# Kernel optimization log

Measured on AMD Instinct MI355X. Metric: run time of the kernel, lower is better.

The kernel has to match this reference:

```python
import jax, jax.numpy as jnp
import numpy as np

NUM_HEADS = 12
KEEP_RATE = 0.7


def setup_inputs() -> dict:
    key = jax.random.key(0)
    ks = jax.random.split(key, 5)
    B, N, C = 64, 197, 768
    x = jax.random.normal(ks[0], (B, N, C), dtype=jnp.float32)
    qkv_w = jax.random.normal(ks[1], (3 * C, C), dtype=jnp.float32) * (C ** -0.5)
    qkv_b = jax.random.normal(ks[2], (3 * C,), dtype=jnp.float32) * 0.02
    proj_w = jax.random.normal(ks[3], (C, C), dtype=jnp.float32) * (C ** -0.5)
    proj_b = jax.random.normal(ks[4], (C,), dtype=jnp.float32) * 0.02
    return {"x": x, "qkv_w": qkv_w, "qkv_b": qkv_b, "proj_w": proj_w, "proj_b": proj_b}


def reference(x, qkv_w, qkv_b, proj_w, proj_b):
    B, N, C = x.shape
    H = NUM_HEADS
    D = C // H
    scale = D ** -0.5
    # qkv projection: [B,N,3C] -> [3,B,H,N,D]
    qkv = (x @ qkv_w.T + qkv_b).reshape(B, N, 3, H, D).transpose(2, 0, 3, 1, 4)
    q, k, v = qkv[0], qkv[1], qkv[2]
    # full materialized attention (required for cls-row extraction)
    attn = jax.nn.softmax(jnp.einsum('bhqd,bhkd->bhqk', q, k) * scale, axis=-1)
    out = jnp.einsum('bhqk,bhkd->bqhd', attn, v).reshape(B, N, C)
    out = out @ proj_w.T + proj_b
    # EViT token pruning: cls-token attention over non-cls keys, head-averaged
    left_tokens = int(KEEP_RATE * (N - 1))  # 137
    cls_attn = attn[:, :, 0, 1:].mean(axis=1)  # [B, N-1]
    _, idx = jax.lax.top_k(cls_attn, left_tokens)  # sorted descending, like torch.topk
    index = jnp.broadcast_to(idx[:, :, None], (B, left_tokens, C))
    return (out, index, idx, cls_attn)
```

## Files before the change

### kernel.cpp

```cpp
#include <hip/hip_runtime.h>
#include <hip/hip_bf16.h>
#include <stdint.h>

constexpr int BATCH = 64;
constexpr int NTOK  = 197;
constexpr int CDIM  = 768;
constexpr int NH    = 12;
constexpr int HD    = 64;
constexpr int MROWS = BATCH * NTOK;
constexpr int MPAD  = 12800;
constexpr int NROWT = MPAD / 128;
constexpr int LEFT  = 137;
constexpr int KPAD  = 224;
constexpr int BH    = BATCH * NH;
constexpr int SPAD  = 208;

constexpr size_t OUT_OFF_OUT   = 0;
constexpr size_t OUT_OFF_INDEX = (size_t)BATCH * NTOK * CDIM;
constexpr size_t OUT_OFF_IDX   = OUT_OFF_INDEX + (size_t)BATCH * LEFT * CDIM;
constexpr size_t OUT_OFF_CLS   = OUT_OFF_IDX + (size_t)BATCH * LEFT;

constexpr size_t WS_CLSPH = 0;
constexpr size_t WS_CLSF  = WS_CLSPH + (size_t)BH * (NTOK - 1);
constexpr size_t WS_IDXI  = WS_CLSF  + (size_t)BATCH * (NTOK - 1);
constexpr size_t WS_Q0    = WS_IDXI  + (size_t)BATCH * LEFT;
constexpr size_t WS_XB    = WS_Q0  + (size_t)BATCH * CDIM;
constexpr size_t WS_WB    = WS_XB  + (size_t)MPAD * CDIM / 2;
constexpr size_t WS_PB    = WS_WB  + (size_t)3 * CDIM * CDIM / 2;
constexpr size_t WS_QB    = WS_PB  + (size_t)CDIM * CDIM / 2;
constexpr size_t WS_KB    = WS_QB  + (size_t)BH * NTOK * HD / 2;
constexpr size_t WS_VTB   = WS_KB  + (size_t)BH * NTOK * HD / 2;
constexpr size_t WS_AOB   = WS_VTB + (size_t)BH * HD * KPAD / 2;
constexpr size_t WS_U     = WS_AOB + (size_t)MPAD * CDIM / 2;
constexpr size_t WS_S     = WS_U   + (size_t)BH * CDIM;

typedef __attribute__((ext_vector_type(8))) short short8;
typedef __attribute__((ext_vector_type(4))) float floatx4;

__device__ __forceinline__ ushort f2bf(float x) {
    __hip_bfloat16 h = __float2bfloat16(x);
    return *(ushort*)&h;
}

__device__ __forceinline__ void load_lds16(const ushort* g, ushort* l) {
    __builtin_amdgcn_global_load_lds(
        (const __attribute__((address_space(1))) uint32_t*)(uintptr_t)g,
        (__attribute__((address_space(3))) uint32_t*)(uint32_t)(uintptr_t)l,
        16, 0, 0);
}

constexpr int X_N4  = MROWS * CDIM / 4;
constexpr int X_NP4 = MPAD * CDIM / 4;
constexpr int W_N4  = 3 * CDIM * CDIM / 4;
constexpr int P_N4  = CDIM * CDIM / 4;
constexpr int CAST_TOTAL = X_NP4 + W_N4 + P_N4;

__global__ __launch_bounds__(256) void cast_all_kernel(const float* __restrict__ x,
                                                       const float* __restrict__ qkv_w,
                                                       const float* __restrict__ proj_w,
                                                       ushort* __restrict__ xb,
                                                       ushort* __restrict__ wb,
                                                       ushort* __restrict__ pb) {
    int i = blockIdx.x * 256 + threadIdx.x;
    const float* src;
    ushort* dst;
    int j, valid;
    if (i < X_NP4) {
        src = x; dst = xb; j = i; valid = (j < X_N4);
    } else if (i < X_NP4 + W_N4) {
        src = qkv_w; dst = wb; j = i - X_NP4; valid = 1;
    } else if (i < CAST_TOTAL) {
        src = proj_w; dst = pb; j = i - X_NP4 - W_N4; valid = 1;
    } else {
        return;
    }
    ushort4 h4 = make_ushort4(0, 0, 0, 0);
    if (valid) {
        float4 a = ((const float4*)src)[j];
        h4 = make_ushort4(f2bf(a.x), f2bf(a.y), f2bf(a.z), f2bf(a.w));
    }
    ((ushort4*)dst)[j] = h4;
}

__global__ __launch_bounds__(256) void q0_kernel(const float* __restrict__ x,
                                                 const float* __restrict__ qkv_w,
                                                 const float* __restrict__ qkv_b,
                                                 float* __restrict__ q0) {
    int tid = blockIdx.x * 256 + threadIdx.x;
    if (tid >= BATCH * CDIM) return;
    int b = tid / CDIM, c = tid - b * CDIM;
    const float* xr = x + (size_t)b * NTOK * CDIM;
    const float* wr = qkv_w + (size_t)c * CDIM;
    float s = 0.f;
    for (int k = 0; k < CDIM; k += 4) {
        float4 xv = *(const float4*)(xr + k);
        float4 wv = *(const float4*)(wr + k);
        s += xv.x * wv.x + xv.y * wv.y + xv.z * wv.z + xv.w * wv.w;
    }
    q0[tid] = s + qkv_b[c];
}

__global__ __launch_bounds__(256) void u_kernel(const float* __restrict__ q0,
                                                const float* __restrict__ qkv_w,
                                                float* __restrict__ U) {
    const int bh = blockIdx.x;
    const int b  = bh / NH;
    const int h  = bh - b * NH;
    const int t  = threadIdx.x;

    __shared__ float q0s[HD];
    if (t < HD) q0s[t] = q0[(size_t)b * CDIM + h * HD + t];
    __syncthreads();

    const float* wk = qkv_w + (size_t)(CDIM + h * HD) * CDIM;
    float a0 = 0.f, a1 = 0.f, a2 = 0.f;
    for (int d = 0; d < HD; d++) {
        const float qd = q0s[d];
        const float* row = wk + (size_t)d * CDIM;
        a0 = fmaf(qd, row[t],       a0);
        a1 = fmaf(qd, row[t + 256], a1);
        a2 = fmaf(qd, row[t + 512], a2);
    }
    float* ub = U + (size_t)bh * CDIM;
    ub[t] = a0; ub[t + 256] = a1; ub[t + 512] = a2;
}

__global__ __launch_bounds__(256) void score_kernel(const float* __restrict__ x,
                                                    const float* __restrict__ U,
                                                    float* __restrict__ S) {
    const int wv   = threadIdx.x >> 6;
    const int lane = threadIdx.x & 63;
    const int j    = blockIdx.x * 4 + wv;
    const int b    = blockIdx.y;
    if (j >= NTOK) return;

    const float* xr = x + ((size_t)b * NTOK + j) * CDIM;
    float4 xv[3];
#pragma unroll
    for (int i = 0; i < 3; i++) xv[i] = *(const float4*)(xr + lane * 4 + i * 256);

    for (int h = 0; h < NH; h++) {
        const float* ur = U + (size_t)(b * NH + h) * CDIM;
        float s = 0.f;
#pragma unroll
        for (int i = 0; i < 3; i++) {
            float4 uv = *(const float4*)(ur + lane * 4 + i * 256);
            s += xv[i].x * uv.x + xv[i].y * uv.y + xv[i].z * uv.z + xv[i].w * uv.w;
        }
#pragma unroll
        for (int off = 32; off >= 1; off >>= 1) s += __shfl_xor(s, off);
        if (lane == 0) S[(size_t)(b * NH + h) * SPAD + j] = s;
    }
}

__global__ __launch_bounds__(64) void cls_softmax_kernel(const float* __restrict__ S,
                                                         const float* __restrict__ q0,
                                                         const float* __restrict__ qkv_b,
                                                         float* __restrict__ CLSPH) {
    const int bh   = blockIdx.x;
    const int b    = bh / NH;
    const int h    = bh - b * NH;
    const int lane = threadIdx.x;

    float qb = q0[(size_t)b * CDIM + h * HD + lane] * qkv_b[CDIM + h * HD + lane];
#pragma unroll
    for (int off = 32; off >= 1; off >>= 1) qb += __shfl_xor(qb, off);

    const float* Sr = S + (size_t)bh * SPAD;
    float sv[4];
    float mloc = -INFINITY;
#pragma unroll
    for (int i = 0; i < 4; i++) {
        const int j = lane + i * 64;
        sv[i] = (j < NTOK) ? (Sr[j] + qb) * 0.125f : -INFINITY;
        mloc = fmaxf(mloc, sv[i]);
    }
#pragma unroll
    for (int off = 32; off >= 1; off >>= 1) mloc = fmaxf(mloc, __shfl_xor(mloc, off));

    float pv[4], ls = 0.f;
#pragma unroll
    for (int i = 0; i < 4; i++) { pv[i] = expf(sv[i] - mloc); ls += pv[i]; }
#pragma unroll
    for (int off = 32; off >= 1; off >>= 1) ls += __shfl_xor(ls, off);

    const float inv = 1.f / ls;
#pragma unroll
    for (int i = 0; i < 4; i++) {
        const int j = lane + i * 64;
        if (j >= 1 && j < NTOK)
            CLSPH[(size_t)bh * (NTOK - 1) + (j - 1)] = pv[i] * inv;
    }
}

template <int MODE, int NCOLT>
__global__ __launch_bounds__(256, 4) void mfma_gemm128(
    const ushort* __restrict__ A, const ushort* __restrict__ W,
    const float* __restrict__ bias,
    float* __restrict__ O0f, ushort* __restrict__ O0q,
    ushort* __restrict__ O1k, ushort* __restrict__ O2vd,
    int Mvalid, int N) {
    constexpr int K   = CDIM;
    constexpr int BK  = 32;
    constexpr int NTK = K / BK;
    __shared__ ushort sA[2 * 128 * BK];
    __shared__ ushort sB[2 * 128 * BK];

    const int t    = threadIdx.x;
    const int lane = t & 63;
    const int w    = t >> 6;
    const int wm   = (w >> 1) * 64;
    const int wn   = (w & 1) * 64;
    const int fr   = lane & 15;
    const int fq   = lane >> 4;
    const int f3   = lane & 3;

    int row, col;
    {
        constexpr int nwg = NROWT * NCOLT;
        constexpr int q = nwg >> 3, r = nwg & 7;
        const int xcd = blockIdx.x & 7, lin = blockIdx.x >> 3;
        const int wg = (xcd < r ? xcd * (q + 1) : r * (q + 1) + (xcd - r) * q) + lin;
        row = wg / NCOLT; col = wg - row * NCOLT;
    }
    const int rowBase = row * 128;
    const int colBase = col * 128;

    auto stage = [&](const ushort* __restrict__ G, ushort* dst, int grow0, int kt) {
#pragma unroll
        for (int i = 0; i < 2; ++i) {
            const int l  = i * 256 + t;
            const int rl = l >> 2;
            const int sl = (l & 3) ^ (rl & 3);
            load_lds16(G + (size_t)(grow0 + rl) * K + kt * BK + sl * 8,
                       dst + l * 8);
        }
    };

    floatx4 acc[4][4];
#pragma unroll
    for (int i = 0; i < 4; ++i)
#pragma unroll
        for (int j = 0; j < 4; ++j)
#pragma unroll
            for (int r2 = 0; r2 < 4; ++r2) acc[i][j][r2] = 0.f;

    const int s0 = (fq ^ f3) * 8;

    stage(A, sA, rowBase, 0);
    stage(W, sB, colBase, 0);

    for (int kt = 0; kt < NTK; ++kt) {
        __syncthreads();
        const int cb = (kt & 1) << 12;
        if (kt + 1 < NTK) {
            stage(A, sA + (cb ^ 4096), rowBase, kt + 1);
            stage(W, sB + (cb ^ 4096), colBase, kt + 1);
        }

        const ushort* pa = sA + cb + (wm + fr) * BK;
        const ushort* pb = sB + cb + (wn + fr) * BK;
        short8 af[4], bf[4];
#pragma unroll
        for (int i = 0; i < 4; ++i) {
            af[i] = *(const short8*)(pa + i * 512 + s0);
            bf[i] = *(const short8*)(pb + i * 512 + s0);
        }
#pragma unroll
        for (int i = 0; i < 4; ++i)
#pragma unroll
            for (int j = 0; j < 4; ++j)
                acc[i][j] = __builtin_amdgcn_mfma_f32_16x16x32_bf16(
                    af[i], bf[j], acc[i][j], 0, 0, 0);
    }

#pragma unroll
    for (int j = 0; j < 4; ++j) {
        const int nn = colBase + wn + j * 16 + fr;
        const float bq = bias[nn];
        if (MODE == 0) {
#pragma unroll
            for (int i = 0; i < 4; ++i) {
                const int mb = rowBase + wm + i * 16 + fq * 4;
#pragma unroll
                for (int r2 = 0; r2 < 4; ++r2) {
                    const int mm = mb + r2;
                    if (mm < Mvalid) O0f[(size_t)mm * N + nn] = acc[i][j][r2] + bq;
                }
            }
        } else {
            const int which = nn / CDIM;
            const int nc    = nn - which * CDIM;
            const int h     = nc >> 6;
            const int d     = nc & 63;
#pragma unroll
            for (int i = 0; i < 4; ++i) {
                const int mb = rowBase + wm + i * 16 + fq * 4;
#pragma unroll
                for (int r2 = 0; r2 < 4; ++r2) {
                    const int mm = mb + r2;
                    if (mm < Mvalid) {
                        const int b   = mm / NTOK;
                        const int tok = mm - b * NTOK;
                        const int bh  = b * NH + h;
                        const ushort val = f2bf(acc[i][j][r2] + bq);
                        if (which == 0)      O0q[((size_t)bh * NTOK + tok) * HD + d] = val;
                        else if (which == 1) O1k[((size_t)bh * NTOK + tok) * HD + d] = val;
                        else                 O2vd[(size_t)mm * CDIM + nc] = val;
                    }
                }
            }
        }
    }
}

__global__ __launch_bounds__(256) void v_transpose_kernel(const ushort* __restrict__ Vd,
                                                          ushort* __restrict__ Vtb) {
    const int bh = blockIdx.x;
    const int b  = bh / NH;
    const int h  = bh - b * NH;
    const int t  = threadIdx.x;

    __shared__ ushort tile[HD][KPAD + 9];

    const int d  = t & 63;
    const int tt = t >> 6;
    const ushort* src = Vd + (size_t)b * NTOK * CDIM + h * HD + d;
    for (int tok0 = 0; tok0 < KPAD; tok0 += 4) {
        const int tok = tok0 + tt;
        ushort v = 0;
        if (tok < NTOK) v = src[(size_t)tok * CDIM];
        tile[d][tok] = v;
    }
    __syncthreads();

    uint* dst = (uint*)(Vtb + (size_t)bh * HD * KPAD);
    constexpr int C2 = KPAD / 2;
    for (int idx = t; idx < HD * C2; idx += 256) {
        const int dd = idx / C2;
        const int c  = idx - dd * C2;
        const uint lo = tile[dd][2 * c];
        const uint hi = tile[dd][2 * c + 1];
        dst[dd * C2 + c] = lo | (hi << 16);
    }
}

__global__ __launch_bounds__(64) void attn_mfma_kernel(const ushort* __restrict__ Qb,
                                                       const ushort* __restrict__ Kb,
                                                       const ushort* __restrict__ Vtb,
                                                       ushort* __restrict__ AOb) {
    const int qt = blockIdx.x;
    const int bh = blockIdx.y;
    const int b  = bh / NH;
    const int h  = bh - b * NH;
    const int lane = threadIdx.x;
    const int qc   = lane & 15;
    const int quad = lane >> 4;

    __shared__ ushort Pl[16][32];
    __shared__ float  alf[16], lf[16];

    const ushort* Qh = Qb  + (size_t)bh * NTOK * HD;
    const ushort* Kh = Kb  + (size_t)bh * NTOK * HD;
    const ushort* Vh = Vtb + (size_t)bh * HD * KPAD;

    const int qrow = min(qt * 16 + qc, NTOK - 1);
    const short8 qf0 = *(const short8*)(Qh + (size_t)qrow * HD + quad * 8);
    const short8 qf1 = *(const short8*)(Qh + (size_t)qrow * HD + 32 + quad * 8);

    floatx4 o[4];
#pragma unroll
    for (int s = 0; s < 4; s++)
#pragma unroll
        for (int r = 0; r < 4; r++) o[s][r] = 0.f;
    float m = -INFINITY, l = 0.f;

    for (int c0 = 0; c0 < NTOK; c0 += 32) {
        const int kr0 = min(c0 + qc, NTOK - 1);
        const int kr1 = min(c0 + 16 + qc, NTOK - 1);
        short8 kf00 = *(const short8*)(Kh + (size_t)kr0 * HD + quad * 8);
        short8 kf01 = *(const short8*)(Kh + (size_t)kr0 * HD + 32 + quad * 8);
        short8 kf10 = *(const short8*)(Kh + (size_t)kr1 * HD + quad * 8);
        short8 kf11 = *(const short8*)(Kh + (size_t)kr1 * HD + 32 + quad * 8);

        floatx4 s0 = {0.f, 0.f, 0.f, 0.f}, s1 = {0.f, 0.f, 0.f, 0.f};
        s0 = __builtin_amdgcn_mfma_f32_16x16x32_bf16(kf00, qf0, s0, 0, 0, 0);
        s0 = __builtin_amdgcn_mfma_f32_16x16x32_bf16(kf01, qf1, s0, 0, 0, 0);
        s1 = __builtin_amdgcn_mfma_f32_16x16x32_bf16(kf10, qf0, s1, 0, 0, 0);
        s1 = __builtin_amdgcn_mfma_f32_16x16x32_bf16(kf11, qf1, s1, 0, 0, 0);

        float sv[8];
        float mloc = -INFINITY;
#pragma unroll
        for (int r = 0; r < 4; r++) {
            const int key0 = c0 + quad * 4 + r;
            const int key1 = key0 + 16;
            sv[r]     = (key0 < NTOK) ? s0[r] * 0.125f : -1e30f;
            sv[4 + r] = (key1 < NTOK) ? s1[r] * 0.125f : -1e30f;
            mloc = fmaxf(mloc, fmaxf(sv[r], sv[4 + r]));
        }
        mloc = fmaxf(mloc, __shfl_xor(mloc, 16));
        mloc = fmaxf(mloc, __shfl_xor(mloc, 32));
        const float mnew  = fmaxf(m, mloc);
        const float alpha = __expf(m - mnew);
        float p[8], ps = 0.f;
#pragma unroll
        for (int i = 0; i < 8; i++) { p[i] = __expf(sv[i] - mnew); ps += p[i]; }
        ps += __shfl_xor(ps, 16);
        ps += __shfl_xor(ps, 32);
        l = l * alpha + ps;
        m = mnew;

#pragma unroll
        for (int r = 0; r < 4; r++) {
            Pl[qc][quad * 4 + r]      = f2bf(p[r]);
            Pl[qc][16 + quad * 4 + r] = f2bf(p[4 + r]);
        }
        if (quad == 0) alf[qc] = alpha;
        __syncthreads();

        float ar[4];
#pragma unroll
        for (int r = 0; r < 4; r++) ar[r] = alf[quad * 4 + r];
#pragma unroll
        for (int s = 0; s < 4; s++)
#pragma unroll
            for (int r = 0; r < 4; r++) o[s][r] *= ar[r];

        const short8 pf = *(const short8*)&Pl[qc][quad * 8];
#pragma unroll
        for (int s = 0; s < 4; s++) {
            const short8 vf = *(const short8*)(Vh + (size_t)(s * 16 + qc) * KPAD + c0 + quad * 8);
            o[s] = __builtin_amdgcn_mfma_f32_16x16x32_bf16(pf, vf, o[s], 0, 0, 0);
        }
        __syncthreads();
    }

    if (quad == 0) lf[qc] = l;
    __syncthreads();

#pragma unroll
    for (int r = 0; r < 4; r++) {
        const int tok = qt * 16 + quad * 4 + r;
        if (tok >= NTOK) continue;
        const float inv = 1.f / lf[quad * 4 + r];
        ushort* dst = AOb + ((size_t)(b * NTOK + tok)) * CDIM + h * HD;
#pragma unroll
        for (int s = 0; s < 4; s++) dst[s * 16 + qc] = f2bf(o[s][r] * inv);
    }
}

__global__ __launch_bounds__(256) void topk_kernel(const float* __restrict__ CLSPH,
                                                   int* __restrict__ idxI,
                                                   float* __restrict__ idxOut,
                                                   float* __restrict__ outCls) {
    const int b = blockIdx.x;
    const int t = threadIdx.x;
    __shared__ float v[NTOK - 1];
    if (t < NTOK - 1) {
        float s = 0.f;
#pragma unroll
        for (int h = 0; h < NH; h++)
            s += CLSPH[(size_t)(b * NH + h) * (NTOK - 1) + t];
        const float val = s * (1.f / 12.f);
        v[t] = val;
        outCls[b * (NTOK - 1) + t] = val;
    }
    __syncthreads();
    if (t < NTOK - 1) {
        float vi = v[t];
        int rank = 0;
        for (int j = 0; j < NTOK - 1; j++) {
            float vj = v[j];
            rank += (vj > vi) || (vj == vi && j < t);
        }
        if (rank < LEFT) {
            idxI[b * LEFT + rank]   = t;
            idxOut[b * LEFT + rank] = (float)t;
        }
    }
}

__global__ void fill_index_kernel(const int* __restrict__ idxI,
                                  float* __restrict__ dst) {
    int tid = blockIdx.x * 256 + threadIdx.x;
    constexpr int C4 = CDIM / 4;
    if (tid >= BATCH * LEFT * C4) return;
    float v = (float)idxI[tid / C4];
    ((float4*)dst)[tid] = make_float4(v, v, v, v);
}

extern "C" void kernel_launch(void* const* d_in, const int* in_sizes, int n_in,
                              void* d_out, int out_size, void* d_ws, size_t ws_size,
                              hipStream_t stream) {
    const float* x      = (const float*)d_in[0];
    const float* qkv_w  = (const float*)d_in[1];
    const float* qkv_b  = (const float*)d_in[2];
    const float* proj_w = (const float*)d_in[3];
    const float* proj_b = (const float*)d_in[4];
    float* out = (float*)d_out;

    float*  ws    = (float*)d_ws;
    float*  clsph = ws + WS_CLSPH;
    int*    idxi  = (int*)(ws + WS_IDXI);
    float*  q0    = ws + WS_Q0;
    ushort* xb    = (ushort*)(ws + WS_XB);
    ushort* wb    = (ushort*)(ws + WS_WB);
    ushort* pb    = (ushort*)(ws + WS_PB);
    ushort* qb    = (ushort*)(ws + WS_QB);
    ushort* kb    = (ushort*)(ws + WS_KB);
    ushort* vtb   = (ushort*)(ws + WS_VTB);
    ushort* aob   = (ushort*)(ws + WS_AOB);
    ushort* vd    = aob;
    float*  U     = ws + WS_U;
    float*  S     = ws + WS_S;

    cast_all_kernel<<<CAST_TOTAL / 256, 256, 0, stream>>>(x, qkv_w, proj_w, xb, wb, pb);

    q0_kernel<<<(BATCH * CDIM + 255) / 256, 256, 0, stream>>>(x, qkv_w, qkv_b, q0);
    u_kernel<<<BH, 256, 0, stream>>>(q0, qkv_w, U);
    score_kernel<<<dim3((NTOK + 3) / 4, BATCH), 256, 0, stream>>>(x, U, S);
    cls_softmax_kernel<<<BH, 64, 0, stream>>>(S, q0, qkv_b, clsph);

    mfma_gemm128<1, 18><<<NROWT * 18, 256, 0, stream>>>(
        xb, wb, qkv_b, nullptr, qb, kb, vd, MROWS, 3 * CDIM);

    v_transpose_kernel<<<BH, 256, 0, stream>>>(vd, vtb);

    attn_mfma_kernel<<<dim3(13, BH), 64, 0, stream>>>(qb, kb, vtb, aob);

    mfma_gemm128<0, 6><<<NROWT * 6, 256, 0, stream>>>(
        aob, pb, proj_b, out + OUT_OFF_OUT, nullptr, nullptr, nullptr,
        MROWS, CDIM);

    topk_kernel<<<BATCH, 256, 0, stream>>>(clsph, idxi, out + OUT_OFF_IDX,
                                           out + OUT_OFF_CLS);

    fill_index_kernel<<<((size_t)BATCH * LEFT * (CDIM / 4) + 255) / 256, 256, 0, stream>>>(
        idxi, out + OUT_OFF_INDEX);
}
```

Measured before the change: 369.9 us.

## Fuse prep kernels, triple-buffer GEMM, write V transposed in epilogue, fuse cls softmax

Merges the bf16 cast, q0 computation and V-transpose padding zeroing into one prep kernel. The QKV GEMM epilogue now writes V directly in transposed layout through LDS, so the separate transpose kernel is gone. The GEMM moves to a 3-stage LDS pipeline with explicit vmcnt waits, drops the LDS swizzle, and lowers its occupancy hint. The cls softmax is folded into the top-k kernel. These changes cut launches and intermediate traffic but may add LDS bank conflicts and uncoalesced transposed stores.

```diff
diff --git a/kernel.cpp b/kernel.cpp
--- a/kernel.cpp
+++ b/kernel.cpp
@@ -54,50 +54,52 @@
 constexpr int W_N4  = 3 * CDIM * CDIM / 4;
 constexpr int P_N4  = CDIM * CDIM / 4;
 constexpr int CAST_TOTAL = X_NP4 + W_N4 + P_N4;
-
-__global__ __launch_bounds__(256) void cast_all_kernel(const float* __restrict__ x,
-                                                       const float* __restrict__ qkv_w,
-                                                       const float* __restrict__ proj_w,
-                                                       ushort* __restrict__ xb,
-                                                       ushort* __restrict__ wb,
-                                                       ushort* __restrict__ pb) {
-    int i = blockIdx.x * 256 + threadIdx.x;
-    const float* src;
-    ushort* dst;
-    int j, valid;
-    if (i < X_NP4) {
-        src = x; dst = xb; j = i; valid = (j < X_N4);
-    } else if (i < X_NP4 + W_N4) {
-        src = qkv_w; dst = wb; j = i - X_NP4; valid = 1;
-    } else if (i < CAST_TOTAL) {
-        src = proj_w; dst = pb; j = i - X_NP4 - W_N4; valid = 1;
+constexpr int CASTB = CAST_TOTAL / 256;
+constexpr int Q0B   = BATCH * CDIM / 256;
+constexpr int PADB  = BH * HD * 16 / 256;
+constexpr int PREPB = CASTB + Q0B + PADB;
+
+__global__ __launch_bounds__(256) void prep_kernel(const float* __restrict__ x,
+                                                   const float* __restrict__ qkv_w,
+                                                   const float* __restrict__ proj_w,
+                                                   const float* __restrict__ qkv_b,
+                                                   ushort* __restrict__ xb,
+                                                   ushort* __restrict__ wb,
+                                                   ushort* __restrict__ pb,
+                                                   float* __restrict__ q0,
+                                                   ushort* __restrict__ vtb) {
+    const int bk = blockIdx.x;
+    const int t  = threadIdx.x;
+    if (bk < CASTB) {
+        const int i = bk * 256 + t;
+        const float* src; ushort* dst; int j, valid;
+        if (i < X_NP4)               { src = x;      dst = xb; j = i;               valid = (j < X_N4); }
+        else if (i < X_NP4 + W_N4)   { src = qkv_w;  dst = wb; j = i - X_NP4;       valid = 1; }
+        else                         { src = proj_w; dst = pb; j = i - X_NP4 - W_N4; valid = 1; }
+        ushort4 h4 = make_ushort4(0, 0, 0, 0);
+        if (valid) {
+            float4 a = ((const float4*)src)[j];
+            h4 = make_ushort4(f2bf(a.x), f2bf(a.y), f2bf(a.z), f2bf(a.w));
+        }
+        ((ushort4*)dst)[j] = h4;
+    } else if (bk < CASTB + Q0B) {
+        const int tid = (bk - CASTB) * 256 + t;
+        const int b = tid / CDIM, c = tid - b * CDIM;
+        const float* xr = x + (size_t)b * NTOK * CDIM;
+        const float* wr = qkv_w + (size_t)c * CDIM;
+        float s = 0.f;
+        for (int k = 0; k < CDIM; k += 4) {
+            float4 xv = *(const float4*)(xr + k);
+            float4 wv = *(const float4*)(wr + k);
+            s += xv.x * wv.x + xv.y * wv.y + xv.z * wv.z + xv.w * wv.w;
+        }
+        q0[tid] = s + qkv_b[c];
     } else {
-        return;
-    }
-    ushort4 h4 = make_ushort4(0, 0, 0, 0);
-    if (valid) {
-        float4 a = ((const float4*)src)[j];
-        h4 = make_ushort4(f2bf(a.x), f2bf(a.y), f2bf(a.z), f2bf(a.w));
-    }
-    ((ushort4*)dst)[j] = h4;
-}
-
-__global__ __launch_bounds__(256) void q0_kernel(const float* __restrict__ x,
-                                                 const float* __restrict__ qkv_w,
-                                                 const float* __restrict__ qkv_b,
-                                                 float* __restrict__ q0) {
-    int tid = blockIdx.x * 256 + threadIdx.x;
-    if (tid >= BATCH * CDIM) return;
-    int b = tid / CDIM, c = tid - b * CDIM;
-    const float* xr = x + (size_t)b * NTOK * CDIM;
-    const float* wr = qkv_w + (size_t)c * CDIM;
-    float s = 0.f;
-    for (int k = 0; k < CDIM; k += 4) {
-        float4 xv = *(const float4*)(xr + k);
-        float4 wv = *(const float4*)(wr + k);
-        s += xv.x * wv.x + xv.y * wv.y + xv.z * wv.z + xv.w * wv.w;
-    }
-    q0[tid] = s + qkv_b[c];
+        const int tid  = (bk - CASTB - Q0B) * 256 + t;
+        const int rowd = tid >> 4;
+        const int c    = tid & 15;
+        ((uint*)vtb)[(size_t)rowd * (KPAD / 2) + 96 + c] = 0u;
+    }
 }
 
 __global__ __launch_bounds__(256) void u_kernel(const float* __restrict__ q0,
@@ -153,58 +155,18 @@
     }
 }
 
-__global__ __launch_bounds__(64) void cls_softmax_kernel(const float* __restrict__ S,
-                                                         const float* __restrict__ q0,
-                                                         const float* __restrict__ qkv_b,
-                                                         float* __restrict__ CLSPH) {
-    const int bh   = blockIdx.x;
-    const int b    = bh / NH;
-    const int h    = bh - b * NH;
-    const int lane = threadIdx.x;
-
-    float qb = q0[(size_t)b * CDIM + h * HD + lane] * qkv_b[CDIM + h * HD + lane];
-#pragma unroll
-    for (int off = 32; off >= 1; off >>= 1) qb += __shfl_xor(qb, off);
-
-    const float* Sr = S + (size_t)bh * SPAD;
-    float sv[4];
-    float mloc = -INFINITY;
-#pragma unroll
-    for (int i = 0; i < 4; i++) {
-        const int j = lane + i * 64;
-        sv[i] = (j < NTOK) ? (Sr[j] + qb) * 0.125f : -INFINITY;
-        mloc = fmaxf(mloc, sv[i]);
-    }
-#pragma unroll
-    for (int off = 32; off >= 1; off >>= 1) mloc = fmaxf(mloc, __shfl_xor(mloc, off));
-
-    float pv[4], ls = 0.f;
-#pragma unroll
-    for (int i = 0; i < 4; i++) { pv[i] = expf(sv[i] - mloc); ls += pv[i]; }
-#pragma unroll
-    for (int off = 32; off >= 1; off >>= 1) ls += __shfl_xor(ls, off);
-
-    const float inv = 1.f / ls;
-#pragma unroll
-    for (int i = 0; i < 4; i++) {
-        const int j = lane + i * 64;
-        if (j >= 1 && j < NTOK)
-            CLSPH[(size_t)bh * (NTOK - 1) + (j - 1)] = pv[i] * inv;
-    }
-}
-
 template <int MODE, int NCOLT>
-__global__ __launch_bounds__(256, 4) void mfma_gemm128(
+__global__ __launch_bounds__(256, 3) void mfma_gemm128(
     const ushort* __restrict__ A, const ushort* __restrict__ W,
     const float* __restrict__ bias,
     float* __restrict__ O0f, ushort* __restrict__ O0q,
-    ushort* __restrict__ O1k, ushort* __restrict__ O2vd,
+    ushort* __restrict__ O1k, ushort* __restrict__ O2vt,
     int Mvalid, int N) {
-    constexpr int K   = CDIM;
-    constexpr int BK  = 32;
-    constexpr int NTK = K / BK;
-    __shared__ ushort sA[2 * 128 * BK];
-    __shared__ ushort sB[2 * 128 * BK];
+    constexpr int K    = CDIM;
+    constexpr int BK   = 32;
+    constexpr int NTK  = K / BK;
+    constexpr int BUFU = 128 * BK;
+    __shared__ ushort smem[6 * BUFU];
 
     const int t    = threadIdx.x;
     const int lane = t & 63;
@@ -213,7 +175,6 @@
     const int wn   = (w & 1) * 64;
     const int fr   = lane & 15;
     const int fq   = lane >> 4;
-    const int f3   = lane & 3;
 
     int row, col;
     {
@@ -231,8 +192,7 @@
         for (int i = 0; i < 2; ++i) {
             const int l  = i * 256 + t;
             const int rl = l >> 2;
-            const int sl = (l & 3) ^ (rl & 3);
-            load_lds16(G + (size_t)(grow0 + rl) * K + kt * BK + sl * 8,
+            load_lds16(G + (size_t)(grow0 + rl) * K + kt * BK + (l & 3) * 8,
                        dst + l * 8);
         }
     };
@@ -245,26 +205,34 @@
 #pragma unroll
             for (int r2 = 0; r2 < 4; ++r2) acc[i][j][r2] = 0.f;
 
-    const int s0 = (fq ^ f3) * 8;
-
-    stage(A, sA, rowBase, 0);
-    stage(W, sB, colBase, 0);
-
-    for (int kt = 0; kt < NTK; ++kt) {
-        __syncthreads();
-        const int cb = (kt & 1) << 12;
-        if (kt + 1 < NTK) {
-            stage(A, sA + (cb ^ 4096), rowBase, kt + 1);
-            stage(W, sB + (cb ^ 4096), colBase, kt + 1);
-        }
-
-        const ushort* pa = sA + cb + (wm + fr) * BK;
-        const ushort* pb = sB + cb + (wn + fr) * BK;
+    const int s0off = fq * 8;
+
+    stage(A, smem + 0 * BUFU, rowBase, 0); stage(W, smem + 3 * BUFU, colBase, 0);
+    stage(A, smem + 1 * BUFU, rowBase, 1); stage(W, smem + 4 * BUFU, colBase, 1);
+    stage(A, smem + 2 * BUFU, rowBase, 2); stage(W, smem + 5 * BUFU, colBase, 2);
+
+    auto iter = [&](int kt, int bi) {
+        if (kt < NTK - 2)       asm volatile("s_waitcnt vmcnt(8)" ::: "memory");
+        else if (kt == NTK - 2) asm volatile("s_waitcnt vmcnt(4)" ::: "memory");
+        else                    asm volatile("s_waitcnt vmcnt(0)" ::: "memory");
+        __builtin_amdgcn_s_barrier();
+        asm volatile("" ::: "memory");
+
+        const ushort* pa = smem + bi * BUFU + (wm + fr) * BK;
+        const ushort* pb = smem + (3 + bi) * BUFU + (wn + fr) * BK;
         short8 af[4], bf[4];
 #pragma unroll
         for (int i = 0; i < 4; ++i) {
-            af[i] = *(const short8*)(pa + i * 512 + s0);
-            bf[i] = *(const short8*)(pb + i * 512 + s0);
+            af[i] = *(const short8*)(pa + i * 512 + s0off);
+            bf[i] = *(const short8*)(pb + i * 512 + s0off);
+        }
+        asm volatile("s_waitcnt lgkmcnt(0)" ::: "memory");
+        __builtin_amdgcn_sched_barrier(0);
+        __builtin_amdgcn_s_barrier();
+        asm volatile("" ::: "memory");
+        if (kt + 3 < NTK) {
+            stage(A, smem + bi * BUFU,       rowBase, kt + 3);
+            stage(W, smem + (3 + bi) * BUFU, colBase, kt + 3);
         }
 #pragma unroll
         for (int i = 0; i < 4; ++i)
@@ -272,13 +240,17 @@
             for (int j = 0; j < 4; ++j)
                 acc[i][j] = __builtin_amdgcn_mfma_f32_16x16x32_bf16(
                     af[i], bf[j], acc[i][j], 0, 0, 0);
-    }
-
-#pragma unroll
-    for (int j = 0; j < 4; ++j) {
-        const int nn = colBase + wn + j * 16 + fr;
-        const float bq = bias[nn];
-        if (MODE == 0) {
+    };
+
+    for (int k0 = 0; k0 < NTK; k0 += 3) {
+        iter(k0, 0); iter(k0 + 1, 1); iter(k0 + 2, 2);
+    }
+
+    if (MODE == 0) {
+#pragma unroll
+        for (int j = 0; j < 4; ++j) {
+            const int nn = colBase + wn + j * 16 + fr;
+            const float bq = bias[nn];
 #pragma unroll
             for (int i = 0; i < 4; ++i) {
                 const int mb = rowBase + wm + i * 16 + fq * 4;
@@ -288,60 +260,68 @@
                     if (mm < Mvalid) O0f[(size_t)mm * N + nn] = acc[i][j][r2] + bq;
                 }
             }
-        } else {
-            const int which = nn / CDIM;
-            const int nc    = nn - which * CDIM;
-            const int h     = nc >> 6;
-            const int d     = nc & 63;
-#pragma unroll
-            for (int i = 0; i < 4; ++i) {
-                const int mb = rowBase + wm + i * 16 + fq * 4;
-#pragma unroll
-                for (int r2 = 0; r2 < 4; ++r2) {
-                    const int mm = mb + r2;
-                    if (mm < Mvalid) {
-                        const int b   = mm / NTOK;
-                        const int tok = mm - b * NTOK;
-                        const int bh  = b * NH + h;
-                        const ushort val = f2bf(acc[i][j][r2] + bq);
-                        if (which == 0)      O0q[((size_t)bh * NTOK + tok) * HD + d] = val;
-                        else if (which == 1) O1k[((size_t)bh * NTOK + tok) * HD + d] = val;
-                        else                 O2vd[(size_t)mm * CDIM + nc] = val;
+        }
+    } else {
+        const int which = colBase / CDIM;
+        if (which < 2) {
+            ushort* O = (which == 0) ? O0q : O1k;
+#pragma unroll
+            for (int j = 0; j < 4; ++j) {
+                const int nn = colBase + wn + j * 16 + fr;
+                const float bq = bias[nn];
+                const int nc = nn - which * CDIM;
+                const int h  = nc >> 6;
+                const int d  = nc & 63;
+#pragma unroll
+                for (int i = 0; i < 4; ++i) {
+                    const int mb = rowBase + wm + i * 16 + fq * 4;
+#pragma unroll
+                    for (int r2 = 0; r2 < 4; ++r2) {
+                        const int mm = mb + r2;
+                        if (mm < Mvalid) {
+                            const int b   = mm / NTOK;
+                            const int tok = mm - b * NTOK;
+                            O[((size_t)(b * NH + h) * NTOK + tok) * HD + d] =
+                                f2bf(acc[i][j][r2] + bq);
+                        }
                     }
                 }
             }
-        }
-    }
-}
-
-__global__ __launch_bounds__(256) void v_transpose_kernel(const ushort* __restrict__ Vd,
-                                                          ushort* __restrict__ Vtb) {
-    const int bh = blockIdx.x;
-    const int b  = bh / NH;
-    const int h  = bh - b * NH;
-    const int t  = threadIdx.x;
-
-    __shared__ ushort tile[HD][KPAD + 9];
-
-    const int d  = t & 63;
-    const int tt = t >> 6;
-    const ushort* src = Vd + (size_t)b * NTOK * CDIM + h * HD + d;
-    for (int tok0 = 0; tok0 < KPAD; tok0 += 4) {
-        const int tok = tok0 + tt;
-        ushort v = 0;
-        if (tok < NTOK) v = src[(size_t)tok * CDIM];
-        tile[d][tok] = v;
-    }
-    __syncthreads();
-
-    uint* dst = (uint*)(Vtb + (size_t)bh * HD * KPAD);
-    constexpr int C2 = KPAD / 2;
-    for (int idx = t; idx < HD * C2; idx += 256) {
-        const int dd = idx / C2;
-        const int c  = idx - dd * C2;
-        const uint lo = tile[dd][2 * c];
-        const uint hi = tile[dd][2 * c + 1];
-        dst[dd * C2 + c] = lo | (hi << 16);
+        } else {
+            const int c0  = colBase - 2 * CDIM;
+            const int h0  = c0 >> 6;
+            ushort* T = smem;
+            const int mhw = wm >> 6;
+#pragma unroll
+            for (int mh = 0; mh < 2; ++mh) {
+                __syncthreads();
+                if (mhw == mh) {
+#pragma unroll
+                    for (int j = 0; j < 4; ++j) {
+                        const int ncl = wn + j * 16 + fr;
+                        const float bq = bias[colBase + ncl];
+#pragma unroll
+                        for (int i = 0; i < 4; ++i)
+#pragma unroll
+                            for (int r2 = 0; r2 < 4; ++r2)
+                                T[(i * 16 + fq * 4 + r2) * 130 + ncl] =
+                                    f2bf(acc[i][j][r2] + bq);
+                    }
+                }
+                __syncthreads();
+                const int mmRow = rowBase + mh * 64 + lane;
+                if (mmRow < Mvalid) {
+                    const int bb  = mmRow / NTOK;
+                    const int tok = mmRow - bb * NTOK;
+                    ushort* vbase = O2vt + ((size_t)(bb * NH + h0) * HD) * KPAD + tok;
+#pragma unroll
+                    for (int s2 = 0; s2 < 32; ++s2) {
+                        const int dd = w * 32 + s2;
+                        vbase[(size_t)dd * KPAD] = T[lane * 130 + dd];
+                    }
+                }
+            }
+        }
     }
 }
 
@@ -450,28 +430,65 @@
     }
 }
 
-__global__ __launch_bounds__(256) void topk_kernel(const float* __restrict__ CLSPH,
-                                                   int* __restrict__ idxI,
-                                                   float* __restrict__ idxOut,
-                                                   float* __restrict__ outCls) {
-    const int b = blockIdx.x;
-    const int t = threadIdx.x;
-    __shared__ float v[NTOK - 1];
+__global__ __launch_bounds__(256) void topk_fused_kernel(const float* __restrict__ S,
+                                                         const float* __restrict__ q0,
+                                                         const float* __restrict__ qkv_b,
+                                                         int* __restrict__ idxI,
+                                                         float* __restrict__ idxOut,
+                                                         float* __restrict__ outCls) {
+    const int b    = blockIdx.x;
+    const int t    = threadIdx.x;
+    const int lane = t & 63;
+    const int w    = t >> 6;
+
+    __shared__ float qbv[NH];
+    __shared__ float redm[4], reds[4];
+    __shared__ float vsh[NTOK - 1];
+
+    if (w == 0) {
+        for (int h = 0; h < NH; ++h) {
+            float p = q0[(size_t)b * CDIM + h * HD + lane] * qkv_b[CDIM + h * HD + lane];
+#pragma unroll
+            for (int off = 32; off >= 1; off >>= 1) p += __shfl_xor(p, off);
+            if (lane == 0) qbv[h] = p;
+        }
+    }
+    __syncthreads();
+
+    float macc = 0.f;
+    for (int h = 0; h < NH; ++h) {
+        const float qb = qbv[h];
+        const float sv = (t < NTOK) ? (S[(size_t)(b * NH + h) * SPAD + t] + qb) * 0.125f
+                                    : -INFINITY;
+        float mloc = sv;
+#pragma unroll
+        for (int off = 32; off >= 1; off >>= 1) mloc = fmaxf(mloc, __shfl_xor(mloc, off));
+        if (lane == 0) redm[w] = mloc;
+        __syncthreads();
+        const float mx = fmaxf(fmaxf(redm[0], redm[1]), fmaxf(redm[2], redm[3]));
+        const float p = (t < NTOK) ? expf(sv - mx) : 0.f;
+        float ls = p;
+#pragma unroll
+        for (int off = 32; off >= 1; off >>= 1) ls += __shfl_xor(ls, off);
+        if (lane == 0) reds[w] = ls;
+        __syncthreads();
+        const float denom = (reds[0] + reds[1]) + (reds[2] + reds[3]);
+        macc += p / denom;
+        __syncthreads();
+    }
+
+    if (t >= 1 && t < NTOK) {
+        const float val = macc * (1.f / 12.f);
+        vsh[t - 1] = val;
+        outCls[(size_t)b * (NTOK - 1) + (t - 1)] = val;
+    }
+    __syncthreads();
+
     if (t < NTOK - 1) {
-        float s = 0.f;
-#pragma unroll
-        for (int h = 0; h < NH; h++)
-            s += CLSPH[(size_t)(b * NH + h) * (NTOK - 1) + t];
-        const float val = s * (1.f / 12.f);
-        v[t] = val;
-        outCls[b * (NTOK - 1) + t] = val;
-    }
-    __syncthreads();
-    if (t < NTOK - 1) {
-        float vi = v[t];
+        const float vi = vsh[t];
         int rank = 0;
         for (int j = 0; j < NTOK - 1; j++) {
-            float vj = v[j];
+            const float vj = vsh[j];
             rank += (vj > vi) || (vj == vi && j < t);
         }
         if (rank < LEFT) {
@@ -501,7 +518,6 @@
     float* out = (float*)d_out;
 
     float*  ws    = (float*)d_ws;
-    float*  clsph = ws + WS_CLSPH;
     int*    idxi  = (int*)(ws + WS_IDXI);
     float*  q0    = ws + WS_Q0;
     ushort* xb    = (ushort*)(ws + WS_XB);
@@ -511,21 +527,17 @@
     ushort* kb    = (ushort*)(ws + WS_KB);
     ushort* vtb   = (ushort*)(ws + WS_VTB);
     ushort* aob   = (ushort*)(ws + WS_AOB);
-    ushort* vd    = aob;
     float*  U     = ws + WS_U;
     float*  S     = ws + WS_S;
 
-    cast_all_kernel<<<CAST_TOTAL / 256, 256, 0, stream>>>(x, qkv_w, proj_w, xb, wb, pb);
-
-    q0_kernel<<<(BATCH * CDIM + 255) / 256, 256, 0, stream>>>(x, qkv_w, qkv_b, q0);
+    prep_kernel<<<PREPB, 256, 0, stream>>>(x, qkv_w, proj_w, qkv_b,
+                                           xb, wb, pb, q0, vtb);
+
     u_kernel<<<BH, 256, 0, stream>>>(q0, qkv_w, U);
     score_kernel<<<dim3((NTOK + 3) / 4, BATCH), 256, 0, stream>>>(x, U, S);
-    cls_softmax_kernel<<<BH, 64, 0, stream>>>(S, q0, qkv_b, clsph);
 
     mfma_gemm128<1, 18><<<NROWT * 18, 256, 0, stream>>>(
-        xb, wb, qkv_b, nullptr, qb, kb, vd, MROWS, 3 * CDIM);
-
-    v_transpose_kernel<<<BH, 256, 0, stream>>>(vd, vtb);
+        xb, wb, qkv_b, nullptr, qb, kb, vtb, MROWS, 3 * CDIM);
 
     attn_mfma_kernel<<<dim3(13, BH), 64, 0, stream>>>(qb, kb, vtb, aob);
 
@@ -533,8 +545,9 @@
         aob, pb, proj_b, out + OUT_OFF_OUT, nullptr, nullptr, nullptr,
         MROWS, CDIM);
 
-    topk_kernel<<<BATCH, 256, 0, stream>>>(clsph, idxi, out + OUT_OFF_IDX,
-                                           out + OUT_OFF_CLS);
+    topk_fused_kernel<<<BATCH, 256, 0, stream>>>(S, q0, qkv_b, idxi,
+                                                 out + OUT_OFF_IDX,
+                                                 out + OUT_OFF_CLS);
 
     fill_index_kernel<<<((size_t)BATCH * LEFT * (CDIM / 4) + 255) / 256, 256, 0, stream>>>(
         idxi, out + OUT_OFF_INDEX);
```

Result: slower. 472.1 us (+27.7%).
